# Kernel optimization log

Measured on AMD Instinct MI355X. Metric: run time of the kernel, lower is better.

The kernel has to match this reference:

```python
import jax, jax.numpy as jnp
import numpy as np

N = 50000   # nodes
E = 800000  # edges
H = 64      # hidden channels
EPS = 1e-16  # PyG softmax denominator epsilon


def _ptconv(x, pos, src, dst, W_src, W_dst, W_val, W_pos, b_pos):
    """PyG PointTransformerConv: per-edge gather, positional MLP, vector
    attention (segment softmax over edges grouped by dst), scatter-sum.
    edge_index convention: src = j (neighbor), dst = i (center)."""
    a_src = x @ W_src          # [N,H] alpha_j projection
    a_dst = x @ W_dst          # [N,H] alpha_i projection
    v = x @ W_val              # [N,H] values
    # relative positional encoding: pos_nn(pos_i - pos_j), [E,H]
    delta = (pos[dst] - pos[src]) @ W_pos + b_pos
    alpha = a_dst[dst] - a_src[src] + delta           # [E,H]
    # numerically-stable vector softmax over variable-size neighborhoods
    m = jax.lax.stop_gradient(jax.ops.segment_max(alpha, dst, num_segments=N))
    e = jnp.exp(alpha - m[dst])
    s = jax.ops.segment_sum(e, dst, num_segments=N)
    attn = e / (s[dst] + EPS)                         # [E,H]
    return jax.ops.segment_sum(attn * (v[src] + delta), dst, num_segments=N)


def setup_inputs() -> dict:
    key = jax.random.key(0)
    ks = jax.random.split(key, 16)
    x = jax.random.normal(ks[0], (N, 3), dtype=jnp.float32)
    pos = jax.random.normal(ks[1], (N, 3), dtype=jnp.float32)
    edge_index = jax.random.randint(ks[2], (2, E), 0, N)
    batch = jnp.zeros((N,), dtype=jnp.int32)

    def lin(k, i, o):
        return (jax.random.normal(k, (i, o), dtype=jnp.float32)
                * np.float32(1.0 / np.sqrt(i)))

    return {
        "x": x, "pos": pos, "edge_index": edge_index, "batch": batch,
        # conv1 (in=3 -> H)
        "W1_src": lin(ks[3], 3, H), "W1_dst": lin(ks[4], 3, H),
        "W1_val": lin(ks[5], 3, H),
        "W1_pos": lin(ks[6], 3, H), "b1_pos": jnp.zeros((H,), jnp.float32),
        # conv2 (H -> H)
        "W2_src": lin(ks[7], H, H), "W2_dst": lin(ks[8], H, H),
        "W2_val": lin(ks[9], H, H),
        "W2_pos": lin(ks[10], 3, H), "b2_pos": jnp.zeros((H,), jnp.float32),
        # MLP head
        "W_fc1": lin(ks[11], H, H // 2), "b_fc1": jnp.zeros((H // 2,), jnp.float32),
        "W_fc2": lin(ks[12], H // 2, 1), "b_fc2": jnp.zeros((1,), jnp.float32),
    }


def reference(x, pos, edge_index, batch,
              W1_src, W1_dst, W1_val, W1_pos, b1_pos,
              W2_src, W2_dst, W2_val, W2_pos, b2_pos,
              W_fc1, b_fc1, W_fc2, b_fc2):
    src, dst = edge_index[0], edge_index[1]
    h = jax.nn.relu(_ptconv(x, pos, src, dst, W1_src, W1_dst, W1_val, W1_pos, b1_pos))
    h = jax.nn.relu(_ptconv(h, pos, src, dst, W2_src, W2_dst, W2_val, W2_pos, b2_pos))
    h = jax.nn.relu(h @ W_fc1 + b_fc1)
    return h @ W_fc2 + b_fc2  # [N, 1]
```

## Files before the change

kernel.cpp:

```cpp
#include <hip/hip_runtime.h>
#include <hip/hip_fp16.h>
#include <math.h>


#define LOG2E 1.44269504088896340736f

typedef _Float16 hf2 __attribute__((ext_vector_type(2)));
union H2U { __half2 hh; hf2 hf; unsigned u; };

#if defined(__has_builtin)
#if __has_builtin(__builtin_amdgcn_fdot2)
#define HAVE_FDOT2 1
#endif
#endif

__device__ __forceinline__ float fdot2(hf2 a, hf2 b, float c) {
#ifdef HAVE_FDOT2
    return __builtin_amdgcn_fdot2(a, b, c, false);
#else
    return fmaf((float)a.x, (float)b.x, fmaf((float)a.y, (float)b.y, c));
#endif
}

__device__ __forceinline__ float2 pack_payload(float a_plus_c, float vv) {
    float t = fminf(fmaxf(-a_plus_c * LOG2E, -86.6f), 86.6f);
    float E = exp2f(t);
    return make_float2(E, E * vv);
}

__global__ void __launch_bounds__(256) hist_proj1_kernel(
        const int* __restrict__ dst, int* __restrict__ count, int* __restrict__ rank,
        const float* __restrict__ x, const float* __restrict__ pos,
        const float* __restrict__ W1_src, const float* __restrict__ W1_val,
        const float* __restrict__ W1_pos,
        float2* __restrict__ g1, int N, int E) {
    int gtid = blockIdx.x * 256 + threadIdx.x;
    int gsz = gridDim.x * 256;
    for (int e = gtid; e < E; e += gsz)
        rank[e] = atomicAdd(&count[dst[e]], 1);

    int lane = threadIdx.x & 63, wid = threadIdx.x >> 6;
    float ws0 = W1_src[lane], ws1 = W1_src[64 + lane], ws2 = W1_src[128 + lane];
    float wv0 = W1_val[lane], wv1 = W1_val[64 + lane], wv2 = W1_val[128 + lane];
    float wp0 = W1_pos[lane], wp1 = W1_pos[64 + lane], wp2 = W1_pos[128 + lane];
    int nwav = gridDim.x * 4;
    for (int node = blockIdx.x * 4 + wid; node < N; node += nwav) {
        float x0 = x[node * 3 + 0], x1 = x[node * 3 + 1], x2 = x[node * 3 + 2];
        float p0 = pos[node * 3 + 0], p1 = pos[node * 3 + 1], p2 = pos[node * 3 + 2];
        float as = fmaf(x0, ws0, fmaf(x1, ws1, x2 * ws2));
        float vv = fmaf(x0, wv0, fmaf(x1, wv1, x2 * wv2));
        float cc = fmaf(p0, wp0, fmaf(p1, wp1, p2 * wp2));
        g1[node * 64 + lane] = pack_payload(as + cc, vv - cc);
    }
}

__global__ void __launch_bounds__(256) scan_kernel(
        const int* __restrict__ count, int* __restrict__ offsets, int n, int nsb) {
    __shared__ int red[4];
    __shared__ int wpre[4];
    int tid = threadIdx.x, lane = tid & 63, wid = tid >> 6;
    int lim = blockIdx.x * 1024;
    int s = 0;
    for (int i = tid * 4; i < lim; i += 1024) {
        int4 c = *(const int4*)&count[i];
        s += c.x + c.y + c.z + c.w;
    }
    #pragma unroll
    for (int off = 32; off >= 1; off >>= 1) s += __shfl_down(s, off);
    if (lane == 0) red[wid] = s;
    __syncthreads();
    int base = red[0] + red[1] + red[2] + red[3];

    int b4 = lim + tid * 4;
    int4 c = make_int4(0, 0, 0, 0);
    if (b4 + 3 < n) {
        c = *(const int4*)&count[b4];
    } else {
        if (b4 + 0 < n) c.x = count[b4 + 0];
        if (b4 + 1 < n) c.y = count[b4 + 1];
        if (b4 + 2 < n) c.z = count[b4 + 2];
    }
    int tsum = c.x + c.y + c.z + c.w;
    int inc = tsum;
    #pragma unroll
    for (int off = 1; off < 64; off <<= 1) {
        int t2 = __shfl_up(inc, off);
        if (lane >= off) inc += t2;
    }
    if (lane == 63) wpre[wid] = inc;
    __syncthreads();
    int wbase = 0;
    for (int q = 0; q < wid; ++q) wbase += wpre[q];
    int excl = base + wbase + (inc - tsum);
    if (b4 + 0 < n) offsets[b4 + 0] = excl;
    if (b4 + 1 < n) offsets[b4 + 1] = excl + c.x;
    if (b4 + 2 < n) offsets[b4 + 2] = excl + c.x + c.y;
    if (b4 + 3 < n) offsets[b4 + 3] = excl + c.x + c.y + c.z;
    if ((int)blockIdx.x == nsb - 1 && tid == 0)
        offsets[n] = base + wpre[0] + wpre[1] + wpre[2] + wpre[3];
}

__global__ void __launch_bounds__(256) scatter_kernel(
        const int* __restrict__ src, const int* __restrict__ dst,
        const int* __restrict__ rank, const int* __restrict__ offsets,
        int* __restrict__ sorted_src, int E) {
    int e = blockIdx.x * 256 + threadIdx.x;
    if (e < E) sorted_src[offsets[dst[e]] + rank[e]] = src[e];
}

__device__ __forceinline__ float edge_node(
        int node, int laneoff,
        const int* __restrict__ offsets, const int* __restrict__ ss,
        const char* __restrict__ gbase, float dv) {
    int beg = offsets[node], end = offsets[node + 1];
    if (beg >= end) return 0.f;
    float s0 = 0.f, n0 = 0.f, s1 = 0.f, n1 = 0.f;
    int e = beg;
    int aligned = min((beg + 3) & ~3, end);
    for (; e < aligned; ++e) {
        int i0 = __builtin_amdgcn_readfirstlane(ss[e]);
        float2 g0 = *(const float2*)(gbase + (((size_t)(unsigned)i0) << 9) + laneoff);
        s0 += g0.x; n0 += g0.y;
    }
    for (; e + 8 <= end; e += 8) {
        int4 ia = *(const int4*)(ss + e);
        int4 ib = *(const int4*)(ss + e + 4);
        int i0 = __builtin_amdgcn_readfirstlane(ia.x);
        int i1 = __builtin_amdgcn_readfirstlane(ia.y);
        int i2 = __builtin_amdgcn_readfirstlane(ia.z);
        int i3 = __builtin_amdgcn_readfirstlane(ia.w);
        int i4 = __builtin_amdgcn_readfirstlane(ib.x);
        int i5 = __builtin_amdgcn_readfirstlane(ib.y);
        int i6 = __builtin_amdgcn_readfirstlane(ib.z);
        int i7 = __builtin_amdgcn_readfirstlane(ib.w);
        float2 g0 = *(const float2*)(gbase + (((size_t)(unsigned)i0) << 9) + laneoff);
        float2 g1 = *(const float2*)(gbase + (((size_t)(unsigned)i1) << 9) + laneoff);
        float2 g2 = *(const float2*)(gbase + (((size_t)(unsigned)i2) << 9) + laneoff);
        float2 g3 = *(const float2*)(gbase + (((size_t)(unsigned)i3) << 9) + laneoff);
        float2 g4 = *(const float2*)(gbase + (((size_t)(unsigned)i4) << 9) + laneoff);
        float2 g5 = *(const float2*)(gbase + (((size_t)(unsigned)i5) << 9) + laneoff);
        float2 g6 = *(const float2*)(gbase + (((size_t)(unsigned)i6) << 9) + laneoff);
        float2 g7 = *(const float2*)(gbase + (((size_t)(unsigned)i7) << 9) + laneoff);
        s0 += g0.x; n0 += g0.y;
        s1 += g1.x; n1 += g1.y;
        s0 += g2.x; n0 += g2.y;
        s1 += g3.x; n1 += g3.y;
        s0 += g4.x; n0 += g4.y;
        s1 += g5.x; n1 += g5.y;
        s0 += g6.x; n0 += g6.y;
        s1 += g7.x; n1 += g7.y;
    }
    for (; e + 4 <= end; e += 4) {
        int4 ia = *(const int4*)(ss + e);
        int i0 = __builtin_amdgcn_readfirstlane(ia.x);
        int i1 = __builtin_amdgcn_readfirstlane(ia.y);
        int i2 = __builtin_amdgcn_readfirstlane(ia.z);
        int i3 = __builtin_amdgcn_readfirstlane(ia.w);
        float2 g0 = *(const float2*)(gbase + (((size_t)(unsigned)i0) << 9) + laneoff);
        float2 g1 = *(const float2*)(gbase + (((size_t)(unsigned)i1) << 9) + laneoff);
        float2 g2 = *(const float2*)(gbase + (((size_t)(unsigned)i2) << 9) + laneoff);
        float2 g3 = *(const float2*)(gbase + (((size_t)(unsigned)i3) << 9) + laneoff);
        s0 += g0.x; n0 += g0.y;
        s1 += g1.x; n1 += g1.y;
        s0 += g2.x; n0 += g2.y;
        s1 += g3.x; n1 += g3.y;
    }
    for (; e < end; ++e) {
        int i0 = __builtin_amdgcn_readfirstlane(ss[e]);
        float2 g0 = *(const float2*)(gbase + (((size_t)(unsigned)i0) << 9) + laneoff);
        s0 += g0.x; n0 += g0.y;
    }
    float s = s0 + s1;
    float r = __builtin_amdgcn_rcpf(s + 1e-37f);
    return fmaxf(fmaf(n0 + n1, r, dv), 0.f);
}

__global__ void __launch_bounds__(256, 8) e1p2_kernel(
        const float* __restrict__ pos,
        const int* __restrict__ offsets, const int* __restrict__ sorted_src,
        const float2* __restrict__ g1,
        const float* __restrict__ W1_pos, const float* __restrict__ b1_pos,
        const float* __restrict__ W2_src, const float* __restrict__ W2_val,
        const float* __restrict__ W2_pos,
        float2* __restrict__ g2, int N) {
    __shared__ uint4 W4q[16 * 64];
    __shared__ __half hsh[4][64];
    int tid = threadIdx.x, lane = tid & 63, wid = tid >> 6;
    for (int idx = tid; idx < 1024; idx += 256) {
        int q = idx >> 6, c = idx & 63, k = 4 * q;
        H2U s01, s23, v01, v23;
        s01.hh = __floats2half2_rn(W2_src[k * 64 + c], W2_src[(k + 1) * 64 + c]);
        s23.hh = __floats2half2_rn(W2_src[(k + 2) * 64 + c], W2_src[(k + 3) * 64 + c]);
        v01.hh = __floats2half2_rn(W2_val[k * 64 + c], W2_val[(k + 1) * 64 + c]);
        v23.hh = __floats2half2_rn(W2_val[(k + 2) * 64 + c], W2_val[(k + 3) * 64 + c]);
        W4q[idx] = make_uint4(s01.u, s23.u, v01.u, v23.u);
    }
    __syncthreads();

    float w1p0 = W1_pos[lane], w1p1 = W1_pos[64 + lane], w1p2 = W1_pos[128 + lane];
    float bp1 = b1_pos[lane];
    float w2p0 = W2_pos[lane], w2p1 = W2_pos[64 + lane], w2p2 = W2_pos[128 + lane];
    int laneoff = lane * 8;
    int nwav = gridDim.x * 4;

    for (int node = blockIdx.x * 4 + wid; node < N; node += nwav) {
        float p0 = pos[node * 3 + 0], p1 = pos[node * 3 + 1], p2 = pos[node * 3 + 2];
        float dpos = fmaf(p0, w1p0, fmaf(p1, w1p1, p2 * w1p2));
        float hval = edge_node(node, laneoff, offsets, sorted_src,
                               (const char*)g1, dpos + bp1);
        hsh[wid][lane] = __float2half(hval);
        const uint2* hq = (const uint2*)hsh[wid];
        float as = 0.f, vv = 0.f;
        #pragma unroll 4
        for (int q = 0; q < 16; ++q) {
            uint2 hu = hq[q];
            H2U h01, h23; h01.u = hu.x; h23.u = hu.y;
            uint4 wq = W4q[q * 64 + lane];
            H2U a0, a1, b0, b1;
            a0.u = wq.x; a1.u = wq.y; b0.u = wq.z; b1.u = wq.w;
            as = fdot2(h01.hf, a0.hf, as);
            as = fdot2(h23.hf, a1.hf, as);
            vv = fdot2(h01.hf, b0.hf, vv);
            vv = fdot2(h23.hf, b1.hf, vv);
        }
        float cc = fmaf(p0, w2p0, fmaf(p1, w2p1, p2 * w2p2));
        g2[node * 64 + lane] = pack_payload(as + cc, vv - cc);
    }
}

__global__ void __launch_bounds__(256, 8) e2head_kernel(
        const float* __restrict__ pos,
        const int* __restrict__ offsets, const int* __restrict__ sorted_src,
        const float2* __restrict__ g2,
        const float* __restrict__ W2_pos, const float* __restrict__ b2_pos,
        const float* __restrict__ Wfc1, const float* __restrict__ bfc1,
        const float* __restrict__ Wfc2, const float* __restrict__ bfc2,
        float* __restrict__ out, int N) {
    __shared__ unsigned Wf2[1024];
    __shared__ __half hsh[4][64];
    int tid = threadIdx.x, lane = tid & 63, wid = tid >> 6;
    for (int idx = tid; idx < 1024; idx += 256) {
        int kk = idx >> 5, c = idx & 31;
        H2U w;
        w.hh = __floats2half2_rn(Wfc1[(2 * kk) * 32 + c], Wfc1[(2 * kk + 1) * 32 + c]);
        Wf2[idx] = w.u;
    }
    __syncthreads();

    float wp0 = W2_pos[lane], wp1 = W2_pos[64 + lane], wp2 = W2_pos[128 + lane];
    float bp = b2_pos[lane];
    int c = lane & 31, khb = (lane >> 5) * 16;
    float bfc1c = bfc1[c], wfc2c = Wfc2[c], bias2 = bfc2[0];
    int laneoff = lane * 8;
    int nwav = gridDim.x * 4;

    for (int node = blockIdx.x * 4 + wid; node < N; node += nwav) {
        float p0 = pos[node * 3 + 0], p1 = pos[node * 3 + 1], p2 = pos[node * 3 + 2];
        float dpos = fmaf(p0, wp0, fmaf(p1, wp1, p2 * wp2));
        float hval = edge_node(node, laneoff, offsets, sorted_src,
                               (const char*)g2, dpos + bp);
        hsh[wid][lane] = __float2half(hval);
        const hf2* h2 = (const hf2*)hsh[wid];
        float t2 = 0.f;
        #pragma unroll 8
        for (int j = 0; j < 16; ++j) {
            hf2 hk = h2[khb + j];
            H2U w; w.u = Wf2[(khb + j) * 32 + c];
            t2 = fdot2(hk, w.hf, t2);
        }
        t2 += __shfl_down(t2, 32);
        t2 = fmaxf(t2 + bfc1c, 0.f) * wfc2c;
        t2 = (lane < 32) ? t2 : 0.f;
        #pragma unroll
        for (int off = 16; off >= 1; off >>= 1) t2 += __shfl_down(t2, off);
        if (lane == 0) out[node] = t2 + bias2;
    }
}

extern "C" void kernel_launch(void* const* d_in, const int* in_sizes, int n_in,
                              void* d_out, int out_size, void* d_ws, size_t ws_size,
                              hipStream_t stream) {
    const float* x   = (const float*)d_in[0];
    const float* pos = (const float*)d_in[1];
    const int* eidx  = (const int*)d_in[2];
    const float* W1_src = (const float*)d_in[4];
    const float* W1_val = (const float*)d_in[6];
    const float* W1_pos = (const float*)d_in[7];
    const float* b1_pos = (const float*)d_in[8];
    const float* W2_src = (const float*)d_in[9];
    const float* W2_val = (const float*)d_in[11];
    const float* W2_pos = (const float*)d_in[12];
    const float* b2_pos = (const float*)d_in[13];
    const float* W_fc1  = (const float*)d_in[14];
    const float* b_fc1  = (const float*)d_in[15];
    const float* W_fc2  = (const float*)d_in[16];
    const float* b_fc2  = (const float*)d_in[17];

    const int N = in_sizes[0] / 3;
    const int E = in_sizes[2] / 2;
    const int* src = eidx;
    const int* dst = eidx + E;
    const int nsb = (N + 1023) / 1024;

    char* w = (char*)d_ws;
    auto carve = [&](size_t bytes) -> void* {
        void* p = (void*)w;
        w += (bytes + 255) & ~size_t(255);
        return p;
    };
    int*    count      = (int*)carve((size_t)N * 4);
    int*    offsets    = (int*)carve((size_t)(N + 1) * 4);
    int*    rank       = (int*)carve((size_t)E * 4);
    int*    sorted_src = (int*)carve((size_t)E * 4);
    float2* g1         = (float2*)carve((size_t)N * 64 * 8);
    float2* g2         = (float2*)carve((size_t)N * 64 * 8);

    hipMemsetAsync(count, 0, (size_t)N * 4, stream);
    hist_proj1_kernel<<<2048, 256, 0, stream>>>(
        dst, count, rank, x, pos, W1_src, W1_val, W1_pos, g1, N, E);
    scan_kernel<<<nsb, 256, 0, stream>>>(count, offsets, N, nsb);
    scatter_kernel<<<(E + 255) / 256, 256, 0, stream>>>(src, dst, rank, offsets,
                                                        sorted_src, E);
    e1p2_kernel<<<2048, 256, 0, stream>>>(
        pos, offsets, sorted_src, g1, W1_pos, b1_pos, W2_src, W2_val, W2_pos, g2, N);
    e2head_kernel<<<2048, 256, 0, stream>>>(
        pos, offsets, sorted_src, g2, W2_pos, b2_pos,
        W_fc1, b_fc1, W_fc2, b_fc2, (float*)d_out, N);
}
```

Measured before the change: 269.8 us.

## Pack per-node softmax payload as two bf16 values to halve gather traffic

The per-node payload (exp weight and weighted value) drops from two fp32 values to two bf16 halves packed in one 32-bit word, halving the bytes read on every edge gather in both aggregation kernels. The weight matrices used by the per-node projection and the head MLP are also moved from shared memory into registers, and the first edge kernel's occupancy hint is lowered to make room for them. The cost is bf16 rounding in the softmax numerator and denominator sums, which may affect accuracy, plus higher register pressure.

```diff
diff --git a/kernel.cpp b/kernel.cpp
--- a/kernel.cpp
+++ b/kernel.cpp
@@ -22,10 +22,15 @@
 #endif
 }
 
-__device__ __forceinline__ float2 pack_payload(float a_plus_c, float vv) {
-    float t = fminf(fmaxf(-a_plus_c * LOG2E, -86.6f), 86.6f);
+__device__ __forceinline__ unsigned bf16_rn(float x) {
+    unsigned b = __float_as_uint(x);
+    return (b + 0x7FFFu + ((b >> 16) & 1u)) >> 16;
+}
+
+__device__ __forceinline__ unsigned pack_payload(float a_plus_c, float vv) {
+    float t = fminf(fmaxf(-a_plus_c * LOG2E, -86.0f), 86.0f);
     float E = exp2f(t);
-    return make_float2(E, E * vv);
+    return (bf16_rn(E) << 16) | bf16_rn(E * vv);
 }
 
 __global__ void __launch_bounds__(256) hist_proj1_kernel(
@@ -33,7 +38,7 @@
         const float* __restrict__ x, const float* __restrict__ pos,
         const float* __restrict__ W1_src, const float* __restrict__ W1_val,
         const float* __restrict__ W1_pos,
-        float2* __restrict__ g1, int N, int E) {
+        unsigned* __restrict__ g1, int N, int E) {
     int gtid = blockIdx.x * 256 + threadIdx.x;
     int gsz = gridDim.x * 256;
     for (int e = gtid; e < E; e += gsz)
@@ -108,6 +113,11 @@
     if (e < E) sorted_src[offsets[dst[e]] + rank[e]] = src[e];
 }
 
+__device__ __forceinline__ void eacc(unsigned u, float& s, float& n) {
+    s += __uint_as_float(u & 0xFFFF0000u);
+    n += __uint_as_float(u << 16);
+}
+
 __device__ __forceinline__ float edge_node(
         int node, int laneoff,
         const int* __restrict__ offsets, const int* __restrict__ ss,
@@ -119,8 +129,8 @@
     int aligned = min((beg + 3) & ~3, end);
     for (; e < aligned; ++e) {
         int i0 = __builtin_amdgcn_readfirstlane(ss[e]);
-        float2 g0 = *(const float2*)(gbase + (((size_t)(unsigned)i0) << 9) + laneoff);
-        s0 += g0.x; n0 += g0.y;
+        unsigned g0 = *(const unsigned*)(gbase + (((size_t)(unsigned)i0) << 8) + laneoff);
+        eacc(g0, s0, n0);
     }
     for (; e + 8 <= end; e += 8) {
         int4 ia = *(const int4*)(ss + e);
@@ -133,22 +143,22 @@
         int i5 = __builtin_amdgcn_readfirstlane(ib.y);
         int i6 = __builtin_amdgcn_readfirstlane(ib.z);
         int i7 = __builtin_amdgcn_readfirstlane(ib.w);
-        float2 g0 = *(const float2*)(gbase + (((size_t)(unsigned)i0) << 9) + laneoff);
-        float2 g1 = *(const float2*)(gbase + (((size_t)(unsigned)i1) << 9) + laneoff);
-        float2 g2 = *(const float2*)(gbase + (((size_t)(unsigned)i2) << 9) + laneoff);
-        float2 g3 = *(const float2*)(gbase + (((size_t)(unsigned)i3) << 9) + laneoff);
-        float2 g4 = *(const float2*)(gbase + (((size_t)(unsigned)i4) << 9) + laneoff);
-        float2 g5 = *(const float2*)(gbase + (((size_t)(unsigned)i5) << 9) + laneoff);
-        float2 g6 = *(const float2*)(gbase + (((size_t)(unsigned)i6) << 9) + laneoff);
-        float2 g7 = *(const float2*)(gbase + (((size_t)(unsigned)i7) << 9) + laneoff);
-        s0 += g0.x; n0 += g0.y;
-        s1 += g1.x; n1 += g1.y;
-        s0 += g2.x; n0 += g2.y;
-        s1 += g3.x; n1 += g3.y;
-        s0 += g4.x; n0 += g4.y;
-        s1 += g5.x; n1 += g5.y;
-        s0 += g6.x; n0 += g6.y;
-        s1 += g7.x; n1 += g7.y;
+        unsigned g0 = *(const unsigned*)(gbase + (((size_t)(unsigned)i0) << 8) + laneoff);
+        unsigned g1 = *(const unsigned*)(gbase + (((size_t)(unsigned)i1) << 8) + laneoff);
+        unsigned g2 = *(const unsigned*)(gbase + (((size_t)(unsigned)i2) << 8) + laneoff);
+        unsigned g3 = *(const unsigned*)(gbase + (((size_t)(unsigned)i3) << 8) + laneoff);
+        unsigned g4 = *(const unsigned*)(gbase + (((size_t)(unsigned)i4) << 8) + laneoff);
+        unsigned g5 = *(const unsigned*)(gbase + (((size_t)(unsigned)i5) << 8) + laneoff);
+        unsigned g6 = *(const unsigned*)(gbase + (((size_t)(unsigned)i6) << 8) + laneoff);
+        unsigned g7 = *(const unsigned*)(gbase + (((size_t)(unsigned)i7) << 8) + laneoff);
+        eacc(g0, s0, n0);
+        eacc(g1, s1, n1);
+        eacc(g2, s0, n0);
+        eacc(g3, s1, n1);
+        eacc(g4, s0, n0);
+        eacc(g5, s1, n1);
+        eacc(g6, s0, n0);
+        eacc(g7, s1, n1);
     }
     for (; e + 4 <= end; e += 4) {
         int4 ia = *(const int4*)(ss + e);
@@ -156,33 +166,33 @@
         int i1 = __builtin_amdgcn_readfirstlane(ia.y);
         int i2 = __builtin_amdgcn_readfirstlane(ia.z);
         int i3 = __builtin_amdgcn_readfirstlane(ia.w);
-        float2 g0 = *(const float2*)(gbase + (((size_t)(unsigned)i0) << 9) + laneoff);
-        float2 g1 = *(const float2*)(gbase + (((size_t)(unsigned)i1) << 9) + laneoff);
-        float2 g2 = *(const float2*)(gbase + (((size_t)(unsigned)i2) << 9) + laneoff);
-        float2 g3 = *(const float2*)(gbase + (((size_t)(unsigned)i3) << 9) + laneoff);
-        s0 += g0.x; n0 += g0.y;
-        s1 += g1.x; n1 += g1.y;
-        s0 += g2.x; n0 += g2.y;
-        s1 += g3.x; n1 += g3.y;
+        unsigned g0 = *(const unsigned*)(gbase + (((size_t)(unsigned)i0) << 8) + laneoff);
+        unsigned g1 = *(const unsigned*)(gbase + (((size_t)(unsigned)i1) << 8) + laneoff);
+        unsigned g2 = *(const unsigned*)(gbase + (((size_t)(unsigned)i2) << 8) + laneoff);
+        unsigned g3 = *(const unsigned*)(gbase + (((size_t)(unsigned)i3) << 8) + laneoff);
+        eacc(g0, s0, n0);
+        eacc(g1, s1, n1);
+        eacc(g2, s0, n0);
+        eacc(g3, s1, n1);
     }
     for (; e < end; ++e) {
         int i0 = __builtin_amdgcn_readfirstlane(ss[e]);
-        float2 g0 = *(const float2*)(gbase + (((size_t)(unsigned)i0) << 9) + laneoff);
-        s0 += g0.x; n0 += g0.y;
+        unsigned g0 = *(const unsigned*)(gbase + (((size_t)(unsigned)i0) << 8) + laneoff);
+        eacc(g0, s0, n0);
     }
     float s = s0 + s1;
     float r = __builtin_amdgcn_rcpf(s + 1e-37f);
     return fmaxf(fmaf(n0 + n1, r, dv), 0.f);
 }
 
-__global__ void __launch_bounds__(256, 8) e1p2_kernel(
+__global__ void __launch_bounds__(256, 4) e1p2_kernel(
         const float* __restrict__ pos,
         const int* __restrict__ offsets, const int* __restrict__ sorted_src,
-        const float2* __restrict__ g1,
+        const unsigned* __restrict__ g1,
         const float* __restrict__ W1_pos, const float* __restrict__ b1_pos,
         const float* __restrict__ W2_src, const float* __restrict__ W2_val,
         const float* __restrict__ W2_pos,
-        float2* __restrict__ g2, int N) {
+        unsigned* __restrict__ g2, int N) {
     __shared__ uint4 W4q[16 * 64];
     __shared__ __half hsh[4][64];
     int tid = threadIdx.x, lane = tid & 63, wid = tid >> 6;
@@ -196,11 +206,14 @@
         W4q[idx] = make_uint4(s01.u, s23.u, v01.u, v23.u);
     }
     __syncthreads();
+    uint4 Wr[16];
+    #pragma unroll
+    for (int q = 0; q < 16; ++q) Wr[q] = W4q[q * 64 + lane];
 
     float w1p0 = W1_pos[lane], w1p1 = W1_pos[64 + lane], w1p2 = W1_pos[128 + lane];
     float bp1 = b1_pos[lane];
     float w2p0 = W2_pos[lane], w2p1 = W2_pos[64 + lane], w2p2 = W2_pos[128 + lane];
-    int laneoff = lane * 8;
+    int laneoff = lane * 4;
     int nwav = gridDim.x * 4;
 
     for (int node = blockIdx.x * 4 + wid; node < N; node += nwav) {
@@ -211,13 +224,12 @@
         hsh[wid][lane] = __float2half(hval);
         const uint2* hq = (const uint2*)hsh[wid];
         float as = 0.f, vv = 0.f;
-        #pragma unroll 4
+        #pragma unroll
         for (int q = 0; q < 16; ++q) {
             uint2 hu = hq[q];
             H2U h01, h23; h01.u = hu.x; h23.u = hu.y;
-            uint4 wq = W4q[q * 64 + lane];
             H2U a0, a1, b0, b1;
-            a0.u = wq.x; a1.u = wq.y; b0.u = wq.z; b1.u = wq.w;
+            a0.u = Wr[q].x; a1.u = Wr[q].y; b0.u = Wr[q].z; b1.u = Wr[q].w;
             as = fdot2(h01.hf, a0.hf, as);
             as = fdot2(h23.hf, a1.hf, as);
             vv = fdot2(h01.hf, b0.hf, vv);
@@ -231,27 +243,27 @@
 __global__ void __launch_bounds__(256, 8) e2head_kernel(
         const float* __restrict__ pos,
         const int* __restrict__ offsets, const int* __restrict__ sorted_src,
-        const float2* __restrict__ g2,
+        const unsigned* __restrict__ g2,
         const float* __restrict__ W2_pos, const float* __restrict__ b2_pos,
         const float* __restrict__ Wfc1, const float* __restrict__ bfc1,
         const float* __restrict__ Wfc2, const float* __restrict__ bfc2,
         float* __restrict__ out, int N) {
-    __shared__ unsigned Wf2[1024];
     __shared__ __half hsh[4][64];
     int tid = threadIdx.x, lane = tid & 63, wid = tid >> 6;
-    for (int idx = tid; idx < 1024; idx += 256) {
-        int kk = idx >> 5, c = idx & 31;
+    int c = lane & 31, khb = (lane >> 5) * 16;
+    unsigned Wr[16];
+    #pragma unroll
+    for (int j = 0; j < 16; ++j) {
         H2U w;
-        w.hh = __floats2half2_rn(Wfc1[(2 * kk) * 32 + c], Wfc1[(2 * kk + 1) * 32 + c]);
-        Wf2[idx] = w.u;
-    }
-    __syncthreads();
+        w.hh = __floats2half2_rn(Wfc1[(2 * (khb + j)) * 32 + c],
+                                 Wfc1[(2 * (khb + j) + 1) * 32 + c]);
+        Wr[j] = w.u;
+    }
 
     float wp0 = W2_pos[lane], wp1 = W2_pos[64 + lane], wp2 = W2_pos[128 + lane];
     float bp = b2_pos[lane];
-    int c = lane & 31, khb = (lane >> 5) * 16;
     float bfc1c = bfc1[c], wfc2c = Wfc2[c], bias2 = bfc2[0];
-    int laneoff = lane * 8;
+    int laneoff = lane * 4;
     int nwav = gridDim.x * 4;
 
     for (int node = blockIdx.x * 4 + wid; node < N; node += nwav) {
@@ -262,10 +274,10 @@
         hsh[wid][lane] = __float2half(hval);
         const hf2* h2 = (const hf2*)hsh[wid];
         float t2 = 0.f;
-        #pragma unroll 8
+        #pragma unroll
         for (int j = 0; j < 16; ++j) {
             hf2 hk = h2[khb + j];
-            H2U w; w.u = Wf2[(khb + j) * 32 + c];
+            H2U w; w.u = Wr[j];
             t2 = fdot2(hk, w.hf, t2);
         }
         t2 += __shfl_down(t2, 32);
@@ -308,12 +320,12 @@
         w += (bytes + 255) & ~size_t(255);
         return p;
     };
-    int*    count      = (int*)carve((size_t)N * 4);
-    int*    offsets    = (int*)carve((size_t)(N + 1) * 4);
-    int*    rank       = (int*)carve((size_t)E * 4);
-    int*    sorted_src = (int*)carve((size_t)E * 4);
-    float2* g1         = (float2*)carve((size_t)N * 64 * 8);
-    float2* g2         = (float2*)carve((size_t)N * 64 * 8);
+    int*      count      = (int*)carve((size_t)N * 4);
+    int*      offsets    = (int*)carve((size_t)(N + 1) * 4);
+    int*      rank       = (int*)carve((size_t)E * 4);
+    int*      sorted_src = (int*)carve((size_t)E * 4);
+    unsigned* g1         = (unsigned*)carve((size_t)N * 64 * 4);
+    unsigned* g2         = (unsigned*)carve((size_t)N * 64 * 4);
 
     hipMemsetAsync(count, 0, (size_t)N * 4, stream);
     hist_proj1_kernel<<<2048, 256, 0, stream>>>(
```

After: 251.1 us. -6.9%, faster.
